# Performance work log

Measured on AMD Instinct MI355X. Metric: run time of the kernel, lower is better.

Reference implementation:

```python
import jax, jax.numpy as jnp
import numpy as np


def setup_inputs() -> dict:
    key = jax.random.key(0)
    ks = jax.random.split(key, 5)
    B, S, D, L = 16, 256, 768, 32
    return {
        "head": jax.random.normal(ks[0], (B, S, D), dtype=jnp.float32),
        "dep": jax.random.normal(ks[1], (B, S, D), dtype=jnp.float32),
        "label_U_diag": jax.random.normal(ks[2], (L, D), dtype=jnp.float32) * 0.02,
        "label_W": jax.random.normal(ks[3], (L, 2 * D), dtype=jnp.float32) * 0.02,
        "label_b": jax.random.normal(ks[4], (L,), dtype=jnp.float32) * 0.02,
    }


def reference(head, dep, label_U_diag, label_W, label_b):
    # head, dep: [b, s, d]; label_U_diag: [l, d]; label_W: [l, 2d]; label_b: [l]
    d = head.shape[-1]
    # Bilinear term with diagonal U: t1[b,l,i,o] = sum_d head[b,i,d]*U[l,d]*dep[b,o,d]
    t1 = jnp.einsum('bid,ld,bod->blio', head, label_U_diag, dep)
    # Linear term: W @ concat(head_i, dep_o) = W_h @ head_i + W_d @ dep_o
    W_h, W_d = label_W[:, :d], label_W[:, d:]
    t2_h = jnp.einsum('ld,bid->bli', W_h, head)  # [b, l, s]
    t2_d = jnp.einsum('ld,bod->blo', W_d, dep)   # [b, l, s]
    return t1 + t2_h[:, :, :, None] + t2_d[:, :, None, :] + label_b[None, :, None, None]
```

## Files before the change

### kernel.cpp

```cpp
#include <hip/hip_runtime.h>
#include <hip/hip_bf16.h>
#include <stdint.h>


#define B_ 16
#define S_ 256
#define D_ 768
#define L_ 32
#define KQ_ (D_ / 8)
#define NC_ 24

typedef unsigned short ushort_t;
typedef __attribute__((ext_vector_type(4))) float f32x4;
typedef __attribute__((ext_vector_type(8))) short s16x8;

__device__ __forceinline__ unsigned int pack_bf16(float f0, float f1) {
  unsigned int u0 = __builtin_bit_cast(unsigned int, f0) + 0x8000u;
  unsigned int u1 = __builtin_bit_cast(unsigned int, f1) + 0x8000u;
  return __builtin_amdgcn_perm(u1, u0, 0x07060302);
}

__global__ __launch_bounds__(256) void prep_kernel(
    const float* __restrict__ head, const float* __restrict__ dep,
    const float* __restrict__ labelW, ushort_t* __restrict__ depb,
    float* __restrict__ t2h, float* __restrict__ t2d) {
  const int wave = threadIdx.x >> 6;
  const int lane = threadIdx.x & 63;
  const int g = blockIdx.x * 4 + wave;
  const int sel = g >> 10;
  const int idx = g & 1023;
  const int b = idx >> 6;
  const int row0 = (idx & 63) * 4;
  const float* src = sel ? dep : head;
  float* t2x = sel ? t2d : t2h;
  const int d0 = lane * 12;

  float h[4][12];
  const float* rp = src + ((size_t)(b * S_ + row0)) * D_ + d0;
#pragma unroll
  for (int r = 0; r < 4; ++r) {
    float4 v0 = *(const float4*)(rp + (size_t)r * D_);
    float4 v1 = *(const float4*)(rp + (size_t)r * D_ + 4);
    float4 v2 = *(const float4*)(rp + (size_t)r * D_ + 8);
    h[r][0] = v0.x; h[r][1] = v0.y; h[r][2] = v0.z; h[r][3] = v0.w;
    h[r][4] = v1.x; h[r][5] = v1.y; h[r][6] = v1.z; h[r][7] = v1.w;
    h[r][8] = v2.x; h[r][9] = v2.y; h[r][10] = v2.z; h[r][11] = v2.w;
  }
  if (sel) {
    const size_t bb = (size_t)b * (KQ_ * S_ * 8);
    const int m = lane >> 1;
#pragma unroll
    for (int r = 0; r < 4; ++r) {
      const int col = row0 + r;
      unsigned int q0 = pack_bf16(h[r][0], h[r][1]);
      unsigned int q1 = pack_bf16(h[r][2], h[r][3]);
      unsigned int q2 = pack_bf16(h[r][4], h[r][5]);
      unsigned int q3 = pack_bf16(h[r][6], h[r][7]);
      unsigned int q4 = pack_bf16(h[r][8], h[r][9]);
      unsigned int q5 = pack_bf16(h[r][10], h[r][11]);
      if ((lane & 1) == 0) {
        uint4 a = {q0, q1, q2, q3};
        uint2 c = {q4, q5};
        *(uint4*)(depb + bb + ((size_t)(3 * m) * S_ + col) * 8) = a;
        *(uint2*)(depb + bb + ((size_t)(3 * m + 1) * S_ + col) * 8) = c;
      } else {
        uint2 c = {q0, q1};
        uint4 a = {q2, q3, q4, q5};
        *(uint2*)(depb + bb + ((size_t)(3 * m + 1) * S_ + col) * 8 + 4) = c;
        *(uint4*)(depb + bb + ((size_t)(3 * m + 2) * S_ + col) * 8) = a;
      }
    }
  }
  const float* wbase = labelW + sel * D_ + d0;
  for (int c = 0; c < 2; ++c) {
    float v[64];
#pragma unroll
    for (int j = 0; j < 64; ++j) v[j] = 0.f;
    const float* wc = wbase + (size_t)(c * 16) * (2 * D_);
#pragma unroll
    for (int lq = 0; lq < 16; ++lq) {
      const float* wp = wc + (size_t)lq * (2 * D_);
      float4 w0 = *(const float4*)(wp);
      float4 w1 = *(const float4*)(wp + 4);
      float4 w2 = *(const float4*)(wp + 8);
      float w[12] = {w0.x, w0.y, w0.z, w0.w, w1.x, w1.y, w1.z, w1.w,
                     w2.x, w2.y, w2.z, w2.w};
#pragma unroll
      for (int j = 0; j < 12; ++j) {
        v[lq * 4 + 0] += h[0][j] * w[j];
        v[lq * 4 + 1] += h[1][j] * w[j];
        v[lq * 4 + 2] += h[2][j] * w[j];
        v[lq * 4 + 3] += h[3][j] * w[j];
      }
    }
#pragma unroll
    for (int off = 32; off >= 1; off >>= 1) {
      const bool hi = (lane & off) != 0;
#pragma unroll
      for (int k = 0; k < 64; ++k) {
        if (k >= off) continue;
        float send = hi ? v[k] : v[k + off];
        float keep = hi ? v[k + off] : v[k];
        v[k] = keep + __shfl_xor(send, off);
      }
    }
    t2x[((size_t)(b * L_ + c * 16 + (lane >> 2))) * S_ + row0 + (lane & 3)] =
        v[0];
  }
}


#define SWZ(o) ((o) ^ ((((o) >> 10) & 3) << 4))

__global__ __launch_bounds__(256, 2) void main_kernel(
    const float* __restrict__ head, const ushort_t* __restrict__ depb,
    const float* __restrict__ U, const float* __restrict__ bias,
    const float* __restrict__ t2h, const float* __restrict__ t2d,
    float* __restrict__ out) {
  __shared__ __attribute__((aligned(16))) ushort_t As[2 * 4096];
  __shared__ float T2[384];

  const int hw = blockIdx.x;
  const int bid = ((hw & 7) << 7) | (hw >> 3);
  const int ic = bid & 1;
  const int bl = bid >> 1;
  const int l = bl & (L_ - 1);
  const int b = bl >> 5;
  const int ti = ic * 128;
  const int t = threadIdx.x;
  const int lane = t & 63;
  const int wave = t >> 6;
  const int wr = wave >> 1;
  const int wc = wave & 1;

  for (int i = t; i < 384; i += 256)
    T2[i] = (i < 128) ? t2h[((size_t)(b * L_ + l)) * S_ + ti + i]
                      : t2d[((size_t)(b * L_ + l)) * S_ + (i - 128)];
  const float bv = bias[l];

  const int row0 = t >> 2;
  const int kg = t & 3;
  const float* hp0 = head + ((size_t)(b * S_ + ti + row0)) * D_ + kg * 8;
  const float* hp1 = hp0 + (size_t)64 * D_;
  const float* Up = U + (size_t)l * D_ + kg * 8;
  const int awo0s = SWZ((kg * 128 + row0) * 8);
  const int awo1s = awo0s + 512;

  const int aros = SWZ(((lane >> 4) * 128 + (lane & 15)) * 8) + wr * 512;

  const ushort_t* dfb =
      depb + (size_t)b * (KQ_ * S_ * 8) +
      ((size_t)((lane >> 4) * 256 + wc * 128 + (lane & 15))) * 8;

  f32x4 acc[4][8];
#pragma unroll
  for (int i = 0; i < 4; ++i)
#pragma unroll
    for (int j = 0; j < 8; ++j) acc[i][j] = {0.f, 0.f, 0.f, 0.f};

  s16x8 bfA[4], bfB[4];
  s16x8 bfHi[4];

#define LOAD_HU(ku)                                                           \
    float4 h0 = *(const float4*)(hp0 + (ku) * 32);                            \
    float4 h1 = *(const float4*)(hp0 + (ku) * 32 + 4);                        \
    float4 h2 = *(const float4*)(hp1 + (ku) * 32);                            \
    float4 h3 = *(const float4*)(hp1 + (ku) * 32 + 4);                        \
    float4 u0 = *(const float4*)(Up + (ku) * 32);                             \
    float4 u1 = *(const float4*)(Up + (ku) * 32 + 4);

#define PACK_WRITE_A(DST)                                                     \
  {                                                                           \
    uint4 w0, w1;                                                             \
    w0.x = pack_bf16(h0.x * u0.x, h0.y * u0.y);                               \
    w0.y = pack_bf16(h0.z * u0.z, h0.w * u0.w);                               \
    w0.z = pack_bf16(h1.x * u1.x, h1.y * u1.y);                               \
    w0.w = pack_bf16(h1.z * u1.z, h1.w * u1.w);                               \
    w1.x = pack_bf16(h2.x * u0.x, h2.y * u0.y);                               \
    w1.y = pack_bf16(h2.z * u0.z, h2.w * u0.w);                               \
    w1.z = pack_bf16(h3.x * u1.x, h3.y * u1.y);                               \
    w1.w = pack_bf16(h3.z * u1.z, h3.w * u1.w);                               \
    *(uint4*)((DST) + awo0s) = w0;                                            \
    *(uint4*)((DST) + awo1s) = w1;                                            \
  }

#define LOAD_BF4(DSTB, chunk, off)                                            \
  {                                                                           \
    const ushort_t* dfn = dfb + (size_t)(chunk) * 8192;                       \
    _Pragma("unroll") for (int ct = 0; ct < 4; ++ct)                          \
        DSTB[ct] = *(const s16x8*)(dfn + ((off) + ct) * 128);                 \
  }

#define MFMA8(AFB, BFB, CO)                                                   \
  {                                                                           \
    _Pragma("unroll") for (int rt = 0; rt < 4; ++rt)                          \
      _Pragma("unroll") for (int ct = 0; ct < 4; ++ct)                        \
          acc[rt][(CO) + ct] = __builtin_amdgcn_mfma_f32_16x16x32_bf16(       \
              AFB[rt], BFB[ct], acc[rt][(CO) + ct], 0, 0, 0);                 \
  }

  {
    LOAD_HU(0)
    PACK_WRITE_A(As)
    LOAD_BF4(bfA, 0, 0)
    LOAD_BF4(bfHi, 0, 4)
  }
  asm volatile("s_waitcnt lgkmcnt(0)" ::: "memory");
  __builtin_amdgcn_s_barrier();
  __builtin_amdgcn_sched_barrier(0);

#define ITER(PB, BLC, BLN, tcur)                                              \
  {                                                                           \
    int tn = (tcur) + 1;                                                      \
    if (tn == NC_) tn = 0;     \
    LOAD_BF4(BLN, tn, 0)                                                      \
    LOAD_HU(tn)                                                               \
    __builtin_amdgcn_sched_barrier(0);       \
    const ushort_t* pr = As + (PB)*4096;                                      \
    s16x8 af[4];                                                              \
    _Pragma("unroll") for (int rt = 0; rt < 4; ++rt)                          \
        af[rt] = *(const s16x8*)(pr + aros + rt * 128);                       \
    __builtin_amdgcn_s_setprio(1);                                            \
    MFMA8(af, BLC, 0)                                                         \
    MFMA8(af, bfHi, 4)                                                        \
    __builtin_amdgcn_s_setprio(0);                                            \
    __builtin_amdgcn_sched_barrier(0);      \
    LOAD_BF4(bfHi, tn, 4)                                                     \
    PACK_WRITE_A(As + ((PB) ^ 1) * 4096)                                      \
    asm volatile("s_waitcnt lgkmcnt(0)" ::: "memory");                        \
    __builtin_amdgcn_s_barrier();                                             \
    __builtin_amdgcn_sched_barrier(0);                                        \
  }

  for (int tt = 0; tt < NC_; tt += 2) {
    ITER(0, bfA, bfB, tt)
    ITER(1, bfB, bfA, tt + 1)
  }
#undef ITER
#undef LOAD_HU
#undef PACK_WRITE_A
#undef LOAD_BF4
#undef MFMA8

  const int colg = lane & 15;
  const int rgrp = lane >> 4;
  float* ob = out + (((size_t)(b * L_ + l)) * S_ + ti + wr * 64) * S_ + wc * 128;
#pragma unroll
  for (int rt = 0; rt < 4; ++rt) {
    const int r0 = rt * 16 + rgrp * 4;
#pragma unroll
    for (int ct = 0; ct < 8; ++ct) {
      const int c = ct * 16 + colg;
      const float addc = T2[128 + wc * 128 + c] + bv;
      float* p = ob + (size_t)r0 * S_ + c;
#pragma unroll
      for (int r = 0; r < 4; ++r)
        p[(size_t)r * S_] = acc[rt][ct][r] + T2[wr * 64 + r0 + r] + addc;
    }
  }
}

extern "C" void kernel_launch(void* const* d_in, const int* in_sizes, int n_in,
                              void* d_out, int out_size, void* d_ws, size_t ws_size,
                              hipStream_t stream) {
  const float* head = (const float*)d_in[0];
  const float* dep = (const float*)d_in[1];
  const float* U = (const float*)d_in[2];
  const float* W = (const float*)d_in[3];
  const float* bias = (const float*)d_in[4];
  float* out = (float*)d_out;

  ushort_t* depb = (ushort_t*)d_ws;
  float* t2h = (float*)((char*)d_ws + (size_t)B_ * S_ * D_ * 2);
  float* t2d = t2h + (size_t)B_ * L_ * S_;

  prep_kernel<<<512, 256, 0, stream>>>(head, dep, W, depb, t2h, t2d);
  main_kernel<<<B_ * L_ * 2, 256, 0, stream>>>(head, depb, U, bias, t2h, t2d, out);
}
```

Baseline: 219.6 us.

## Give each wave a private A tile to drop block-wide barriers in main loop

Each wave now builds its own copy of the scaled head tile (head times U, packed to bf16) in a private LDS region instead of sharing one block-wide tile. The per-iteration s_barrier goes away and each wave only waits on its own LDS writes. The cost is that the two waves sharing a row group both load and pack the same head rows, which doubles that global traffic and pack work. LDS use also doubles, which may press on occupancy at two blocks per CU.

```diff
diff --git a/kernel.cpp b/kernel.cpp
--- a/kernel.cpp
+++ b/kernel.cpp
@@ -110,14 +110,14 @@
 }
 
 
-#define SWZ(o) ((o) ^ ((((o) >> 10) & 3) << 4))
+#define SWZ(o) ((o) ^ ((((o) >> 9) & 3) << 4))
 
 __global__ __launch_bounds__(256, 2) void main_kernel(
     const float* __restrict__ head, const ushort_t* __restrict__ depb,
     const float* __restrict__ U, const float* __restrict__ bias,
     const float* __restrict__ t2h, const float* __restrict__ t2d,
     float* __restrict__ out) {
-  __shared__ __attribute__((aligned(16))) ushort_t As[2 * 4096];
+  __shared__ __attribute__((aligned(16))) ushort_t As[4 * 2 * 2048];
   __shared__ float T2[384];
 
   const int hw = blockIdx.x;
@@ -136,17 +136,18 @@
   for (int i = t; i < 384; i += 256)
     T2[i] = (i < 128) ? t2h[((size_t)(b * L_ + l)) * S_ + ti + i]
                       : t2d[((size_t)(b * L_ + l)) * S_ + (i - 128)];
+  __syncthreads();
   const float bv = bias[l];
 
-  const int row0 = t >> 2;
-  const int kg = t & 3;
-  const float* hp0 = head + ((size_t)(b * S_ + ti + row0)) * D_ + kg * 8;
-  const float* hp1 = hp0 + (size_t)64 * D_;
-  const float* Up = U + (size_t)l * D_ + kg * 8;
-  const int awo0s = SWZ((kg * 128 + row0) * 8);
-  const int awo1s = awo0s + 512;
-
-  const int aros = SWZ(((lane >> 4) * 128 + (lane & 15)) * 8) + wr * 512;
+  const int q = lane & 3;
+  const int r0 = lane >> 2;
+  const float* hfs =
+      head + ((size_t)(b * S_ + ti + wr * 64 + r0)) * D_ + q * 8;
+  const float* Ups = U + (size_t)l * D_ + q * 8;
+  ushort_t* awb = As + wave * 4096;
+  const int awos = SWZ((q * 64 + r0) * 8);
+
+  const int aros = SWZ(((lane >> 4) * 64 + (lane & 15)) * 8);
 
   const ushort_t* dfb =
       depb + (size_t)b * (KQ_ * S_ * 8) +
@@ -162,27 +163,32 @@
   s16x8 bfHi[4];
 
 #define LOAD_HU(ku)                                                           \
-    float4 h0 = *(const float4*)(hp0 + (ku) * 32);                            \
-    float4 h1 = *(const float4*)(hp0 + (ku) * 32 + 4);                        \
-    float4 h2 = *(const float4*)(hp1 + (ku) * 32);                            \
-    float4 h3 = *(const float4*)(hp1 + (ku) * 32 + 4);                        \
-    float4 u0 = *(const float4*)(Up + (ku) * 32);                             \
-    float4 u1 = *(const float4*)(Up + (ku) * 32 + 4);
+    float4 ha0 = *(const float4*)(hfs + (ku) * 32);                           \
+    float4 ha1 = *(const float4*)(hfs + (ku) * 32 + 4);                       \
+    float4 hb0 = *(const float4*)(hfs + (size_t)16 * D_ + (ku) * 32);         \
+    float4 hb1 = *(const float4*)(hfs + (size_t)16 * D_ + (ku) * 32 + 4);     \
+    float4 hc0 = *(const float4*)(hfs + (size_t)32 * D_ + (ku) * 32);         \
+    float4 hc1 = *(const float4*)(hfs + (size_t)32 * D_ + (ku) * 32 + 4);     \
+    float4 hd0 = *(const float4*)(hfs + (size_t)48 * D_ + (ku) * 32);         \
+    float4 hd1 = *(const float4*)(hfs + (size_t)48 * D_ + (ku) * 32 + 4);     \
+    float4 u0 = *(const float4*)(Ups + (ku) * 32);                            \
+    float4 u1 = *(const float4*)(Ups + (ku) * 32 + 4);
+
+#define PACK_ROW(DST, OFF, x0, x1)                                            \
+  {                                                                           \
+    uint4 w;                                                                  \
+    w.x = pack_bf16((x0).x * u0.x, (x0).y * u0.y);                            \
+    w.y = pack_bf16((x0).z * u0.z, (x0).w * u0.w);                            \
+    w.z = pack_bf16((x1).x * u1.x, (x1).y * u1.y);                            \
+    w.w = pack_bf16((x1).z * u1.z, (x1).w * u1.w);                            \
+    *(uint4*)((DST) + (OFF)) = w;                                             \
+  }
 
 #define PACK_WRITE_A(DST)                                                     \
-  {                                                                           \
-    uint4 w0, w1;                                                             \
-    w0.x = pack_bf16(h0.x * u0.x, h0.y * u0.y);                               \
-    w0.y = pack_bf16(h0.z * u0.z, h0.w * u0.w);                               \
-    w0.z = pack_bf16(h1.x * u1.x, h1.y * u1.y);                               \
-    w0.w = pack_bf16(h1.z * u1.z, h1.w * u1.w);                               \
-    w1.x = pack_bf16(h2.x * u0.x, h2.y * u0.y);                               \
-    w1.y = pack_bf16(h2.z * u0.z, h2.w * u0.w);                               \
-    w1.z = pack_bf16(h3.x * u1.x, h3.y * u1.y);                               \
-    w1.w = pack_bf16(h3.z * u1.z, h3.w * u1.w);                               \
-    *(uint4*)((DST) + awo0s) = w0;                                            \
-    *(uint4*)((DST) + awo1s) = w1;                                            \
-  }
+    PACK_ROW(DST, awos, ha0, ha1)                                             \
+    PACK_ROW(DST, awos + 128, hb0, hb1)                                       \
+    PACK_ROW(DST, awos + 256, hc0, hc1)                                       \
+    PACK_ROW(DST, awos + 384, hd0, hd1)
 
 #define LOAD_BF4(DSTB, chunk, off)                                            \
   {                                                                           \
@@ -200,14 +206,11 @@
   }
 
   {
-    LOAD_HU(0)
-    PACK_WRITE_A(As)
     LOAD_BF4(bfA, 0, 0)
     LOAD_BF4(bfHi, 0, 4)
-  }
-  asm volatile("s_waitcnt lgkmcnt(0)" ::: "memory");
-  __builtin_amdgcn_s_barrier();
-  __builtin_amdgcn_sched_barrier(0);
+    LOAD_HU(0)
+    PACK_WRITE_A(awb)
+  }
 
 #define ITER(PB, BLC, BLN, tcur)                                              \
   {                                                                           \
@@ -216,7 +219,8 @@
     LOAD_BF4(BLN, tn, 0)                                                      \
     LOAD_HU(tn)                                                               \
     __builtin_amdgcn_sched_barrier(0);       \
-    const ushort_t* pr = As + (PB)*4096;                                      \
+    asm volatile("s_waitcnt lgkmcnt(0)" ::: "memory");   \
+    const ushort_t* pr = awb + (PB)*2048;                                     \
     s16x8 af[4];                                                              \
     _Pragma("unroll") for (int rt = 0; rt < 4; ++rt)                          \
         af[rt] = *(const s16x8*)(pr + aros + rt * 128);                       \
@@ -226,10 +230,7 @@
     __builtin_amdgcn_s_setprio(0);                                            \
     __builtin_amdgcn_sched_barrier(0);      \
     LOAD_BF4(bfHi, tn, 4)                                                     \
-    PACK_WRITE_A(As + ((PB) ^ 1) * 4096)                                      \
-    asm volatile("s_waitcnt lgkmcnt(0)" ::: "memory");                        \
-    __builtin_amdgcn_s_barrier();                                             \
-    __builtin_amdgcn_sched_barrier(0);                                        \
+    PACK_WRITE_A(awb + ((PB) ^ 1) * 2048)                                     \
   }
 
   for (int tt = 0; tt < NC_; tt += 2) {
@@ -238,6 +239,7 @@
   }
 #undef ITER
 #undef LOAD_HU
+#undef PACK_ROW
 #undef PACK_WRITE_A
 #undef LOAD_BF4
 #undef MFMA8
@@ -247,15 +249,15 @@
   float* ob = out + (((size_t)(b * L_ + l)) * S_ + ti + wr * 64) * S_ + wc * 128;
 #pragma unroll
   for (int rt = 0; rt < 4; ++rt) {
-    const int r0 = rt * 16 + rgrp * 4;
+    const int r0e = rt * 16 + rgrp * 4;
 #pragma unroll
     for (int ct = 0; ct < 8; ++ct) {
       const int c = ct * 16 + colg;
       const float addc = T2[128 + wc * 128 + c] + bv;
-      float* p = ob + (size_t)r0 * S_ + c;
+      float* p = ob + (size_t)r0e * S_ + c;
 #pragma unroll
       for (int r = 0; r < 4; ++r)
-        p[(size_t)r * S_] = acc[rt][ct][r] + T2[wr * 64 + r0 + r] + addc;
+        p[(size_t)r * S_] = acc[rt][ct][r] + T2[wr * 64 + r0e + r] + addc;
     }
   }
 }
```

Result: slower. 227.2 us (+3.4%).
